# Kernel tuning notes

Hardware: AMD Instinct MI355X
Metric: run time of the kernel (lower is better)

The kernel has to match this reference:

```python
import jax, jax.numpy as jnp
import numpy as np

B, N, E, T, S = 4096, 16, 512, 128, 256  # batch, num_experts, expert_dim, task_dim, scenario_dim


def setup_inputs() -> dict:
    key = jax.random.key(0)
    k1, k2, k3, k4 = jax.random.split(key, 4)
    return {
        "scene_repr": jax.random.normal(k1, (B, S), dtype=jnp.float32),
        "task_anchor": jax.random.normal(k2, (B, T), dtype=jnp.float32),
        "expert_reprs": jax.random.normal(k3, (B, N, E), dtype=jnp.float32),
        "v": jax.random.normal(k4, (E + T, 1), dtype=jnp.float32),
    }


def reference(scene_repr, task_anchor, expert_reprs, v):
    # Original: score_i = concat([expert_i, task_anchor]) @ v for each expert i.
    # Vectorized: split v into expert part and task part; task contribution is
    # identical for every expert, so compute it once and broadcast.
    E_ = expert_reprs.shape[-1]
    v_e = v[:E_, 0]   # [E]
    v_t = v[E_:, 0]   # [T]
    scores = jnp.einsum('bne,e->bn', expert_reprs, v_e) + (task_anchor @ v_t)[:, None]  # [B, N]
    attention_weights = jax.nn.softmax(scores, axis=1)  # [B, N]
    aggregated_repr = jnp.einsum('bne,bn->be', expert_reprs, attention_weights)  # [B, E]
    return aggregated_repr, attention_weights
```

## Files before the change

kernel.cpp:

```cpp
#include <hip/hip_runtime.h>


#define NB 4096
#define NEXP 16
#define EDIM 512

typedef float f32x4 __attribute__((ext_vector_type(4)));

__global__ __launch_bounds__(256, 2) void meta_attn_kernel(
    const float* __restrict__ expert,
    const float* __restrict__ v,
    float* __restrict__ out_agg,
    float* __restrict__ out_w)
{
    const int wave = threadIdx.x >> 6;
    const int lane = threadIdx.x & 63;
    const int b = blockIdx.x * 4 + wave;

    const float* row = expert + (size_t)b * (NEXP * EDIM);

    const f32x4 ve0 = *(const f32x4*)(v + 4 * lane);
    const f32x4 ve1 = *(const f32x4*)(v + 256 + 4 * lane);

    f32x4 tile[NEXP][2];

#pragma unroll
    for (int n = 0; n < NEXP; ++n) {
        tile[n][0] = __builtin_nontemporal_load(
            (const f32x4*)(row + n * EDIM + 4 * lane));
        tile[n][1] = __builtin_nontemporal_load(
            (const f32x4*)(row + n * EDIM + 256 + 4 * lane));
    }

    float s[NEXP];
#pragma unroll
    for (int n = 0; n < NEXP; ++n) {
        const f32x4 a = tile[n][0];
        const f32x4 c = tile[n][1];
        s[n] = a.x * ve0.x + a.y * ve0.y + a.z * ve0.z + a.w * ve0.w
             + c.x * ve1.x + c.y * ve1.y + c.z * ve1.z + c.w * ve1.w;
    }

#pragma unroll
    for (int n = 0; n < NEXP; ++n) {
        float x = s[n];
#pragma unroll
        for (int m = 1; m < 64; m <<= 1)
            x += __shfl_xor(x, m, 64);
        s[n] = x;
    }

    float mx = s[0];
#pragma unroll
    for (int n = 1; n < NEXP; ++n) mx = fmaxf(mx, s[n]);
    float w[NEXP];
    float sum = 0.0f;
#pragma unroll
    for (int n = 0; n < NEXP; ++n) {
        w[n] = __expf(s[n] - mx);
        sum += w[n];
    }
    const float inv = 1.0f / sum;
#pragma unroll
    for (int n = 0; n < NEXP; ++n) w[n] *= inv;

    f32x4 acc0 = {0.f, 0.f, 0.f, 0.f};
    f32x4 acc1 = {0.f, 0.f, 0.f, 0.f};
#pragma unroll
    for (int n = 0; n < NEXP; ++n) {
        const float wn = w[n];
        acc0 += wn * tile[n][0];
        acc1 += wn * tile[n][1];
    }

    __builtin_nontemporal_store(acc0, (f32x4*)(out_agg + (size_t)b * EDIM + 4 * lane));
    __builtin_nontemporal_store(acc1, (f32x4*)(out_agg + (size_t)b * EDIM + 256 + 4 * lane));

#pragma unroll
    for (int n = 0; n < NEXP; ++n)
        if (lane == n) out_w[(size_t)b * NEXP + n] = w[n];
}

extern "C" void kernel_launch(void* const* d_in, const int* in_sizes, int n_in,
                              void* d_out, int out_size, void* d_ws, size_t ws_size,
                              hipStream_t stream) {
    const float* expert = (const float*)d_in[2];
    const float* v      = (const float*)d_in[3];
    float* out_agg = (float*)d_out;
    float* out_w   = (float*)d_out + (size_t)NB * EDIM;

    meta_attn_kernel<<<dim3(NB / 4), dim3(256), 0, stream>>>(expert, v, out_agg, out_w);
}
```

Baseline: 27.60 us.

## Re-read expert rows in second pass instead of holding tile in registers

The kernel no longer keeps all 16x8 floats of the expert tile in registers. It loads them in chunks of four experts to compute scores, then re-reads the same rows (expected to hit cache) for the weighted sum. Launch bounds are raised to 4 blocks per CU so more waves are resident to hide memory latency. The weight store becomes a single predicated store per lane. The trade-off is a second read of 32KB per row from L2/MALL and more global load instructions.

```diff
diff --git a/kernel.cpp b/kernel.cpp
--- a/kernel.cpp
+++ b/kernel.cpp
@@ -7,7 +7,7 @@
 
 typedef float f32x4 __attribute__((ext_vector_type(4)));
 
-__global__ __launch_bounds__(256, 2) void meta_attn_kernel(
+__global__ __launch_bounds__(256, 4) void meta_attn_kernel(
     const float* __restrict__ expert,
     const float* __restrict__ v,
     float* __restrict__ out_agg,
@@ -22,23 +22,23 @@
     const f32x4 ve0 = *(const f32x4*)(v + 4 * lane);
     const f32x4 ve1 = *(const f32x4*)(v + 256 + 4 * lane);
 
-    f32x4 tile[NEXP][2];
+    float s[NEXP];
 
 #pragma unroll
-    for (int n = 0; n < NEXP; ++n) {
-        tile[n][0] = __builtin_nontemporal_load(
-            (const f32x4*)(row + n * EDIM + 4 * lane));
-        tile[n][1] = __builtin_nontemporal_load(
-            (const f32x4*)(row + n * EDIM + 256 + 4 * lane));
-    }
-
-    float s[NEXP];
+    for (int c = 0; c < 4; ++c) {
+        f32x4 a[4], d[4];
 #pragma unroll
-    for (int n = 0; n < NEXP; ++n) {
-        const f32x4 a = tile[n][0];
-        const f32x4 c = tile[n][1];
-        s[n] = a.x * ve0.x + a.y * ve0.y + a.z * ve0.z + a.w * ve0.w
-             + c.x * ve1.x + c.y * ve1.y + c.z * ve1.z + c.w * ve1.w;
+        for (int k = 0; k < 4; ++k) {
+            const int n = c * 4 + k;
+            a[k] = *(const f32x4*)(row + n * EDIM + 4 * lane);
+            d[k] = *(const f32x4*)(row + n * EDIM + 256 + 4 * lane);
+        }
+#pragma unroll
+        for (int k = 0; k < 4; ++k) {
+            const int n = c * 4 + k;
+            s[n] = a[k].x * ve0.x + a[k].y * ve0.y + a[k].z * ve0.z + a[k].w * ve0.w
+                 + d[k].x * ve1.x + d[k].y * ve1.y + d[k].z * ve1.z + d[k].w * ve1.w;
+        }
     }
 
 #pragma unroll
@@ -64,21 +64,34 @@
 #pragma unroll
     for (int n = 0; n < NEXP; ++n) w[n] *= inv;
 
+    asm volatile("" ::: "memory");
+
     f32x4 acc0 = {0.f, 0.f, 0.f, 0.f};
     f32x4 acc1 = {0.f, 0.f, 0.f, 0.f};
 #pragma unroll
-    for (int n = 0; n < NEXP; ++n) {
-        const float wn = w[n];
-        acc0 += wn * tile[n][0];
-        acc1 += wn * tile[n][1];
+    for (int c = 0; c < 4; ++c) {
+        f32x4 a[4], d[4];
+#pragma unroll
+        for (int k = 0; k < 4; ++k) {
+            const int n = c * 4 + k;
+            a[k] = __builtin_nontemporal_load((const f32x4*)(row + n * EDIM + 4 * lane));
+            d[k] = __builtin_nontemporal_load((const f32x4*)(row + n * EDIM + 256 + 4 * lane));
+        }
+#pragma unroll
+        for (int k = 0; k < 4; ++k) {
+            const int n = c * 4 + k;
+            acc0 += w[n] * a[k];
+            acc1 += w[n] * d[k];
+        }
     }
 
     __builtin_nontemporal_store(acc0, (f32x4*)(out_agg + (size_t)b * EDIM + 4 * lane));
     __builtin_nontemporal_store(acc1, (f32x4*)(out_agg + (size_t)b * EDIM + 256 + 4 * lane));
 
+    float myw = w[0];
 #pragma unroll
-    for (int n = 0; n < NEXP; ++n)
-        if (lane == n) out_w[(size_t)b * NEXP + n] = w[n];
+    for (int n = 1; n < NEXP; ++n) myw = (lane == n) ? w[n] : myw;
+    if (lane < NEXP) out_w[(size_t)b * NEXP + lane] = myw;
 }
 
 extern "C" void kernel_launch(void* const* d_in, const int* in_sizes, int n_in,
```

Result: slower. 43.16 us (+56.4%).
